# Performance work log

Hardware: AMD Instinct MI355X
Metric: run time of the kernel (lower is better)

Reference implementation:

```python
import jax, jax.numpy as jnp
import numpy as np

EPS = 1e-8  # torch.nn.CosineSimilarity default eps
SCALE_WEIGHT = (1.0, 2.0, 3.0, 4.0)  # weight[idx] for 4 scales


def _nearest_labels(lab, H, W):
    # torch F.interpolate mode='nearest': src_idx = floor(dst_idx * in/out)
    H0, W0 = lab.shape[2], lab.shape[3]
    ri = (jnp.arange(H) * H0) // H
    ci = (jnp.arange(W) * W0) // W
    return lab[:, :, ri][:, :, :, ci]


def _scale_loss(pseudo_labels, feat, feat_old, num_class, num_old_class):
    B, C, H, W = feat.shape
    lab = _nearest_labels(pseudo_labels, H, W).reshape(-1)          # [B*H*W]
    f = jnp.transpose(feat, (0, 2, 3, 1)).reshape(-1, C)            # (b h w) c
    fo = jnp.transpose(feat_old, (0, 2, 3, 1)).reshape(-1, C)
    nf = jnp.maximum(jnp.sqrt(jnp.sum(f * f, axis=1)), EPS)
    nfo = jnp.maximum(jnp.sqrt(jnp.sum(fo * fo, axis=1)), EPS)
    sim = jnp.sum(f * fo, axis=1) / (nf * nfo)                      # per-pixel cosine
    # segment-reduce by class; label 255 (ignore) is out-of-range and dropped
    seg = jax.ops.segment_sum(sim, lab, num_segments=num_class)
    cnt = jax.ops.segment_sum(jnp.ones_like(sim), lab, num_segments=num_class)
    mean_sim = seg / jnp.maximum(cnt, 1.0)
    cls = jnp.arange(num_class)
    factor = jnp.where(cls == 0, num_old_class / num_class,
                       jnp.where(cls <= num_old_class, 1.0, 0.0))
    present = cnt > 0
    dis = 1.0 - mean_sim
    return jnp.sum(jnp.where(present, factor * dis, 0.0))


def setup_inputs() -> dict:
    key = jax.random.key(0)
    ks = jax.random.split(key, 9)
    B, C = 8, 256
    sizes = [(128, 128), (64, 64), (32, 32), (16, 16)]
    inp = {
        "pseudo_labels": jax.random.randint(ks[0], (B, 1, 512, 512), 0, 21, dtype=jnp.int64)
        if jax.config.jax_enable_x64 else
        jax.random.randint(ks[0], (B, 1, 512, 512), 0, 21).astype(jnp.int32),
    }
    for i, (h, w) in enumerate(sizes):
        inp[f"f{i}"] = jax.random.normal(ks[1 + i], (B, C, h, w), dtype=jnp.float32)
        inp[f"fo{i}"] = jax.random.normal(ks[5 + i], (B, C, h, w), dtype=jnp.float32)
    inp["num_class"] = 21
    inp["num_old_class"] = 15
    return inp


def reference(pseudo_labels, f0, f1, f2, f3, fo0, fo1, fo2, fo3, num_class, num_old_class):
    feats = (f0, f1, f2, f3)
    feats_old = (fo0, fo1, fo2, fo3)
    loss = jnp.float32(0.0)
    for idx in range(4):
        loss = loss + SCALE_WEIGHT[idx] * _scale_loss(
            pseudo_labels, feats[idx], feats_old[idx], num_class, num_old_class)
    return loss
```

## Files before the change

### kernel.cpp

```cpp
#include <hip/hip_runtime.h>
#include <math.h>


#define EPSV 1e-8f

__global__ __launch_bounds__(512)
void msrd_main(const float* __restrict__ f0, const float* __restrict__ fo0,
               const float* __restrict__ f1, const float* __restrict__ fo1,
               const float* __restrict__ f2, const float* __restrict__ fo2,
               const float* __restrict__ f3, const float* __restrict__ fo3,
               const int*   __restrict__ labels,
               const int*   __restrict__ p_nclass,
               float* __restrict__ ws)
{
    int bid = blockIdx.x;
    int scale, lb, logW, logHW, sshift;
    const float *f, *fo;
    if (bid < 512)      { scale = 0; lb = bid;       f = f0; fo = fo0; logW = 7; logHW = 14; sshift = 2; }
    else if (bid < 640) { scale = 1; lb = bid - 512; f = f1; fo = fo1; logW = 6; logHW = 12; sshift = 3; }
    else if (bid < 672) { scale = 2; lb = bid - 640; f = f2; fo = fo2; logW = 5; logHW = 10; sshift = 4; }
    else                { scale = 3; lb = bid - 672; f = f3; fo = fo3; logW = 4; logHW = 8;  sshift = 5; }
    const int HW = 1 << logHW;
    const int W  = 1 << logW;

    const int tid  = threadIdx.x;
    const int wave = tid >> 6;
    const int lane = tid & 63;

    const int g   = lb * 64 + lane;
    const int pix = g << 2;
    const int b   = pix >> logHW;
    const int rem = pix & (HW - 1);

    const int c0 = wave * 32;
    const float4* __restrict__ fp  = (const float4*)(f  + (size_t)(b * 256 + c0) * HW + rem);
    const float4* __restrict__ fop = (const float4*)(fo + (size_t)(b * 256 + c0) * HW + rem);
    const int str4 = HW >> 2;

    float dx=0.f,dy=0.f,dz=0.f,dw=0.f;
    float ax=0.f,ay=0.f,az=0.f,aw=0.f;
    float bx=0.f,by=0.f,bz=0.f,bw=0.f;
    #pragma unroll 4
    for (int c = 0; c < 32; ++c) {
        float4 x = fp[c * str4];
        float4 y = fop[c * str4];
        dx = fmaf(x.x, y.x, dx); dy = fmaf(x.y, y.y, dy);
        dz = fmaf(x.z, y.z, dz); dw = fmaf(x.w, y.w, dw);
        ax = fmaf(x.x, x.x, ax); ay = fmaf(x.y, x.y, ay);
        az = fmaf(x.z, x.z, az); aw = fmaf(x.w, x.w, aw);
        bx = fmaf(y.x, y.x, bx); by = fmaf(y.y, y.y, by);
        bz = fmaf(y.z, y.z, bz); bw = fmaf(y.w, y.w, bw);
    }

    __shared__ float4 sD[8][64], sA[8][64], sB[8][64];
    __shared__ float bin_sim[32], bin_cnt[32];
    if (tid < 32) { bin_sim[tid] = 0.f; bin_cnt[tid] = 0.f; }
    sD[wave][lane] = make_float4(dx,dy,dz,dw);
    sA[wave][lane] = make_float4(ax,ay,az,aw);
    sB[wave][lane] = make_float4(bx,by,bz,bw);
    __syncthreads();

    if (wave == 0) {
        float4 D = sD[0][lane], A = sA[0][lane], Bv = sB[0][lane];
        #pragma unroll
        for (int w = 1; w < 8; ++w) {
            float4 t;
            t = sD[w][lane]; D.x += t.x; D.y += t.y; D.z += t.z; D.w += t.w;
            t = sA[w][lane]; A.x += t.x; A.y += t.y; A.z += t.z; A.w += t.w;
            t = sB[w][lane]; Bv.x += t.x; Bv.y += t.y; Bv.z += t.z; Bv.w += t.w;
        }
        const int nclass  = *p_nclass;
        const int labbase = b << 18;
        float Dv[4] = {D.x, D.y, D.z, D.w};
        float Av[4] = {A.x, A.y, A.z, A.w};
        float Bw[4] = {Bv.x, Bv.y, Bv.z, Bv.w};
        #pragma unroll
        for (int j = 0; j < 4; ++j) {
            float na  = fmaxf(sqrtf(Av[j]), EPSV);
            float nb  = fmaxf(sqrtf(Bw[j]), EPSV);
            float sim = Dv[j] / (na * nb);
            int p    = rem + j;
            int h    = p >> logW;
            int col  = p & (W - 1);
            int lidx = labbase + ((h << sshift) << 9) + (col << sshift);
            int lab  = labels[lidx];
            if ((unsigned)lab < (unsigned)nclass) {
                atomicAdd(&bin_sim[lab], sim);
                atomicAdd(&bin_cnt[lab], 1.0f);
            }
        }
    }
    __syncthreads();

    if (tid < 32) {
        float s = bin_sim[tid], c = bin_cnt[tid];
        if (s != 0.f || c != 0.f) {
            atomicAdd(&ws[scale * 64 + tid],      s);
            atomicAdd(&ws[scale * 64 + 32 + tid], c);
        }
    }
}

__global__ void msrd_final(const float* __restrict__ ws,
                           const int* __restrict__ p_nclass,
                           const int* __restrict__ p_nold,
                           float* __restrict__ out)
{
    if (threadIdx.x == 0 && blockIdx.x == 0) {
        const int nc = *p_nclass;
        const int no = *p_nold;
        const float wgt[4] = {1.f, 2.f, 3.f, 4.f};
        float loss = 0.f;
        for (int s = 0; s < 4; ++s) {
            float sl = 0.f;
            for (int c = 0; c < nc && c < 32; ++c) {
                float seg = ws[s * 64 + c];
                float cnt = ws[s * 64 + 32 + c];
                if (cnt > 0.f) {
                    float factor = (c == 0) ? (float)no / (float)nc
                                            : (c <= no ? 1.f : 0.f);
                    sl += factor * (1.f - seg / fmaxf(cnt, 1.f));
                }
            }
            loss += wgt[s] * sl;
        }
        out[0] = loss;
    }
}

extern "C" void kernel_launch(void* const* d_in, const int* in_sizes, int n_in,
                              void* d_out, int out_size, void* d_ws, size_t ws_size,
                              hipStream_t stream) {
    const int*   labels = (const int*)  d_in[0];
    const float* f0  = (const float*)d_in[1];
    const float* fo0 = (const float*)d_in[2];
    const float* f1  = (const float*)d_in[3];
    const float* fo1 = (const float*)d_in[4];
    const float* f2  = (const float*)d_in[5];
    const float* fo2 = (const float*)d_in[6];
    const float* f3  = (const float*)d_in[7];
    const float* fo3 = (const float*)d_in[8];
    const int* p_nclass = (const int*)d_in[9];
    const int* p_nold   = (const int*)d_in[10];
    float* out = (float*)d_out;
    float* ws  = (float*)d_ws;

    hipMemsetAsync(ws, 0, 4 * 64 * sizeof(float), stream);
    msrd_main<<<dim3(680), dim3(512), 0, stream>>>(f0, fo0, f1, fo1, f2, fo2, f3, fo3,
                                                   labels, p_nclass, ws);
    msrd_final<<<dim3(1), dim3(64), 0, stream>>>(ws, p_nclass, p_nold, out);
}
```

Baseline: 360.8 us.

## Split channels across half-waves and batch loads for more parallelism

Each block now covers 128 pixels instead of 256, and the grid grows to 1360 blocks. Each half-wave takes 16 of a wave's 32 channels, and the two halves are combined with a cross-lane shuffle. The loads are issued in batches of eight float4 per tensor before the FMAs to raise memory-level parallelism. The cost is a row segment per channel that is half as long, so less contiguous bytes per access, plus more blocks and more global atomics.

```diff
diff --git a/kernel.cpp b/kernel.cpp
--- a/kernel.cpp
+++ b/kernel.cpp
@@ -16,58 +16,79 @@
     int bid = blockIdx.x;
     int scale, lb, logW, logHW, sshift;
     const float *f, *fo;
-    if (bid < 512)      { scale = 0; lb = bid;       f = f0; fo = fo0; logW = 7; logHW = 14; sshift = 2; }
-    else if (bid < 640) { scale = 1; lb = bid - 512; f = f1; fo = fo1; logW = 6; logHW = 12; sshift = 3; }
-    else if (bid < 672) { scale = 2; lb = bid - 640; f = f2; fo = fo2; logW = 5; logHW = 10; sshift = 4; }
-    else                { scale = 3; lb = bid - 672; f = f3; fo = fo3; logW = 4; logHW = 8;  sshift = 5; }
+    if (bid < 1024)      { scale = 0; lb = bid;        f = f0; fo = fo0; logW = 7; logHW = 14; sshift = 2; }
+    else if (bid < 1280) { scale = 1; lb = bid - 1024; f = f1; fo = fo1; logW = 6; logHW = 12; sshift = 3; }
+    else if (bid < 1344) { scale = 2; lb = bid - 1280; f = f2; fo = fo2; logW = 5; logHW = 10; sshift = 4; }
+    else                 { scale = 3; lb = bid - 1344; f = f3; fo = fo3; logW = 4; logHW = 8;  sshift = 5; }
     const int HW = 1 << logHW;
     const int W  = 1 << logW;
 
     const int tid  = threadIdx.x;
     const int wave = tid >> 6;
     const int lane = tid & 63;
+    const int half = lane >> 5;
+    const int gi   = lane & 31;
 
-    const int g   = lb * 64 + lane;
+    const int g   = lb * 32 + gi;
     const int pix = g << 2;
     const int b   = pix >> logHW;
     const int rem = pix & (HW - 1);
 
-    const int c0 = wave * 32;
-    const float4* __restrict__ fp  = (const float4*)(f  + (size_t)(b * 256 + c0) * HW + rem);
-    const float4* __restrict__ fop = (const float4*)(fo + (size_t)(b * 256 + c0) * HW + rem);
-    const int str4 = HW >> 2;
+    const int c0 = wave * 32 + half * 16;
+    const float* __restrict__ fpb  = f  + (((size_t)(b * 256 + c0)) << logHW) + rem;
+    const float* __restrict__ fopb = fo + (((size_t)(b * 256 + c0)) << logHW) + rem;
 
     float dx=0.f,dy=0.f,dz=0.f,dw=0.f;
     float ax=0.f,ay=0.f,az=0.f,aw=0.f;
     float bx=0.f,by=0.f,bz=0.f,bw=0.f;
-    #pragma unroll 4
-    for (int c = 0; c < 32; ++c) {
-        float4 x = fp[c * str4];
-        float4 y = fop[c * str4];
-        dx = fmaf(x.x, y.x, dx); dy = fmaf(x.y, y.y, dy);
-        dz = fmaf(x.z, y.z, dz); dw = fmaf(x.w, y.w, dw);
-        ax = fmaf(x.x, x.x, ax); ay = fmaf(x.y, x.y, ay);
-        az = fmaf(x.z, x.z, az); aw = fmaf(x.w, x.w, aw);
-        bx = fmaf(y.x, y.x, bx); by = fmaf(y.y, y.y, by);
-        bz = fmaf(y.z, y.z, bz); bw = fmaf(y.w, y.w, bw);
+
+    #pragma unroll
+    for (int batch = 0; batch < 2; ++batch) {
+        float4 X[8], Y[8];
+        const size_t cb = (size_t)(batch * 8) << logHW;
+        #pragma unroll
+        for (int j = 0; j < 8; ++j)
+            X[j] = *(const float4*)(fpb + cb + ((size_t)j << logHW));
+        #pragma unroll
+        for (int j = 0; j < 8; ++j)
+            Y[j] = *(const float4*)(fopb + cb + ((size_t)j << logHW));
+        #pragma unroll
+        for (int j = 0; j < 8; ++j) {
+            float4 x = X[j], y = Y[j];
+            dx = fmaf(x.x, y.x, dx); dy = fmaf(x.y, y.y, dy);
+            dz = fmaf(x.z, y.z, dz); dw = fmaf(x.w, y.w, dw);
+            ax = fmaf(x.x, x.x, ax); ay = fmaf(x.y, x.y, ay);
+            az = fmaf(x.z, x.z, az); aw = fmaf(x.w, x.w, aw);
+            bx = fmaf(y.x, y.x, bx); by = fmaf(y.y, y.y, by);
+            bz = fmaf(y.z, y.z, bz); bw = fmaf(y.w, y.w, bw);
+        }
     }
 
-    __shared__ float4 sD[8][64], sA[8][64], sB[8][64];
+    dx += __shfl_xor(dx, 32); dy += __shfl_xor(dy, 32);
+    dz += __shfl_xor(dz, 32); dw += __shfl_xor(dw, 32);
+    ax += __shfl_xor(ax, 32); ay += __shfl_xor(ay, 32);
+    az += __shfl_xor(az, 32); aw += __shfl_xor(aw, 32);
+    bx += __shfl_xor(bx, 32); by += __shfl_xor(by, 32);
+    bz += __shfl_xor(bz, 32); bw += __shfl_xor(bw, 32);
+
+    __shared__ float4 sD[8][32], sA[8][32], sB[8][32];
     __shared__ float bin_sim[32], bin_cnt[32];
     if (tid < 32) { bin_sim[tid] = 0.f; bin_cnt[tid] = 0.f; }
-    sD[wave][lane] = make_float4(dx,dy,dz,dw);
-    sA[wave][lane] = make_float4(ax,ay,az,aw);
-    sB[wave][lane] = make_float4(bx,by,bz,bw);
+    if (half == 0) {
+        sD[wave][gi] = make_float4(dx,dy,dz,dw);
+        sA[wave][gi] = make_float4(ax,ay,az,aw);
+        sB[wave][gi] = make_float4(bx,by,bz,bw);
+    }
     __syncthreads();
 
-    if (wave == 0) {
-        float4 D = sD[0][lane], A = sA[0][lane], Bv = sB[0][lane];
+    if (tid < 32) {
+        float4 D = sD[0][gi], A = sA[0][gi], Bv = sB[0][gi];
         #pragma unroll
         for (int w = 1; w < 8; ++w) {
             float4 t;
-            t = sD[w][lane]; D.x += t.x; D.y += t.y; D.z += t.z; D.w += t.w;
-            t = sA[w][lane]; A.x += t.x; A.y += t.y; A.z += t.z; A.w += t.w;
-            t = sB[w][lane]; Bv.x += t.x; Bv.y += t.y; Bv.z += t.z; Bv.w += t.w;
+            t = sD[w][gi]; D.x += t.x; D.y += t.y; D.z += t.z; D.w += t.w;
+            t = sA[w][gi]; A.x += t.x; A.y += t.y; A.z += t.z; A.w += t.w;
+            t = sB[w][gi]; Bv.x += t.x; Bv.y += t.y; Bv.z += t.z; Bv.w += t.w;
         }
         const int nclass  = *p_nclass;
         const int labbase = b << 18;
@@ -146,7 +167,7 @@
     float* ws  = (float*)d_ws;
 
     hipMemsetAsync(ws, 0, 4 * 64 * sizeof(float), stream);
-    msrd_main<<<dim3(680), dim3(512), 0, stream>>>(f0, fo0, f1, fo1, f2, fo2, f3, fo3,
-                                                   labels, p_nclass, ws);
+    msrd_main<<<dim3(1360), dim3(512), 0, stream>>>(f0, fo0, f1, fo1, f2, fo2, f3, fo3,
+                                                    labels, p_nclass, ws);
     msrd_final<<<dim3(1), dim3(64), 0, stream>>>(ws, p_nclass, p_nold, out);
 }
```

Result: no change. 360.5 us (-0.1%).

## Stream feature channels through double-buffered LDS via global_load_lds

Applied to the files above, without the earlier changes.

Each block now covers 256 pixels with one thread per pixel. Feature channels are streamed in 8-channel chunks into double-buffered shared memory using direct global-to-LDS loads, and the next chunk is issued while the current one is consumed. The chunk start is rotated per block so blocks spread over different channel regions. This removes the cross-wave partial-sum reduction and overlaps memory latency with compute, at the cost of a barrier per chunk and smaller 256-thread blocks.

```diff
diff --git a/kernel.cpp b/kernel.cpp
--- a/kernel.cpp
+++ b/kernel.cpp
@@ -4,7 +4,14 @@
 
 #define EPSV 1e-8f
 
-__global__ __launch_bounds__(512)
+typedef const __attribute__((address_space(1))) void GV;
+typedef __attribute__((address_space(3))) void LV;
+
+__device__ __forceinline__ void gl_lds16(const float* gp, float* lp) {
+    __builtin_amdgcn_global_load_lds((GV*)gp, (LV*)lp, 16, 0, 0);
+}
+
+__global__ __launch_bounds__(256)
 void msrd_main(const float* __restrict__ f0, const float* __restrict__ fo0,
                const float* __restrict__ f1, const float* __restrict__ fo1,
                const float* __restrict__ f2, const float* __restrict__ fo2,
@@ -13,92 +20,91 @@
                const int*   __restrict__ p_nclass,
                float* __restrict__ ws)
 {
-    int bid = blockIdx.x;
-    int scale, lb, logW, logHW, sshift;
+    const int bid = blockIdx.x;
+    int scale, win, logW, logHW, sshift;
     const float *f, *fo;
-    if (bid < 512)      { scale = 0; lb = bid;       f = f0; fo = fo0; logW = 7; logHW = 14; sshift = 2; }
-    else if (bid < 640) { scale = 1; lb = bid - 512; f = f1; fo = fo1; logW = 6; logHW = 12; sshift = 3; }
-    else if (bid < 672) { scale = 2; lb = bid - 640; f = f2; fo = fo2; logW = 5; logHW = 10; sshift = 4; }
-    else                { scale = 3; lb = bid - 672; f = f3; fo = fo3; logW = 4; logHW = 8;  sshift = 5; }
-    const int HW = 1 << logHW;
-    const int W  = 1 << logW;
+    if (bid < 512)      { scale = 0; win = bid;       f = f0; fo = fo0; logW = 7; logHW = 14; sshift = 2; }
+    else if (bid < 640) { scale = 1; win = bid - 512; f = f1; fo = fo1; logW = 6; logHW = 12; sshift = 3; }
+    else if (bid < 672) { scale = 2; win = bid - 640; f = f2; fo = fo2; logW = 5; logHW = 10; sshift = 4; }
+    else                { scale = 3; win = bid - 672; f = f3; fo = fo3; logW = 4; logHW = 8;  sshift = 5; }
+    const int W = 1 << logW;
 
     const int tid  = threadIdx.x;
     const int wave = tid >> 6;
     const int lane = tid & 63;
 
-    const int g   = lb * 64 + lane;
-    const int pix = g << 2;
-    const int b   = pix >> logHW;
-    const int rem = pix & (HW - 1);
+    const int pxbase = win << 8;
+    const int b      = pxbase >> logHW;
+    const int wrem   = pxbase & ((1 << logHW) - 1);
 
-    const int c0 = wave * 32;
-    const float4* __restrict__ fp  = (const float4*)(f  + (size_t)(b * 256 + c0) * HW + rem);
-    const float4* __restrict__ fop = (const float4*)(fo + (size_t)(b * 256 + c0) * HW + rem);
-    const int str4 = HW >> 2;
+    __shared__ float lds[2][16][256];
+    __shared__ float bin_sim[32], bin_cnt[32];
+    if (tid < 32) { bin_sim[tid] = 0.f; bin_cnt[tid] = 0.f; }
 
-    float dx=0.f,dy=0.f,dz=0.f,dw=0.f;
-    float ax=0.f,ay=0.f,az=0.f,aw=0.f;
-    float bx=0.f,by=0.f,bz=0.f,bw=0.f;
-    #pragma unroll 4
-    for (int c = 0; c < 32; ++c) {
-        float4 x = fp[c * str4];
-        float4 y = fop[c * str4];
-        dx = fmaf(x.x, y.x, dx); dy = fmaf(x.y, y.y, dy);
-        dz = fmaf(x.z, y.z, dz); dw = fmaf(x.w, y.w, dw);
-        ax = fmaf(x.x, x.x, ax); ay = fmaf(x.y, x.y, ay);
-        az = fmaf(x.z, x.z, az); aw = fmaf(x.w, x.w, aw);
-        bx = fmaf(y.x, y.x, bx); by = fmaf(y.y, y.y, by);
-        bz = fmaf(y.z, y.z, bz); bw = fmaf(y.w, y.w, bw);
+    const size_t img_off = ((size_t)(b << 8)) << logHW;
+
+    const int   p0    = wave * 4;
+    const float* base0 = (p0 < 8) ? f : fo;
+    (void)base0;
+
+    float dot = 0.f, na2 = 0.f, nb2 = 0.f;
+
+    #define ISSUE(s, buf)                                                        \
+        {                                                                        \
+            const int chunk = ((s) + bid) & 31;                                  \
+            _Pragma("unroll")                                                    \
+            for (int k = 0; k < 4; ++k) {                                        \
+                const int p  = p0 + k;                                           \
+                const float* tb = (p < 8) ? f : fo;                              \
+                const int ch = chunk * 8 + (p & 7);                              \
+                const float* gp = tb + img_off + (((size_t)ch) << logHW)         \
+                                   + wrem + lane * 4;                            \
+                gl_lds16(gp, &lds[(buf)][p][0]);                                 \
+            }                                                                    \
+        }
+
+    ISSUE(0, 0);
+    __syncthreads();
+
+    #pragma unroll 1
+    for (int s = 0; s < 32; ++s) {
+        const int buf = s & 1;
+        if (s < 31) ISSUE(s + 1, buf ^ 1);
+        #pragma unroll
+        for (int c = 0; c < 8; ++c) {
+            const float x = lds[buf][c][tid];
+            const float y = lds[buf][8 + c][tid];
+            dot = fmaf(x, y, dot);
+            na2 = fmaf(x, x, na2);
+            nb2 = fmaf(y, y, nb2);
+        }
+        __syncthreads();
     }
 
-    __shared__ float4 sD[8][64], sA[8][64], sB[8][64];
-    __shared__ float bin_sim[32], bin_cnt[32];
-    if (tid < 32) { bin_sim[tid] = 0.f; bin_cnt[tid] = 0.f; }
-    sD[wave][lane] = make_float4(dx,dy,dz,dw);
-    sA[wave][lane] = make_float4(ax,ay,az,aw);
-    sB[wave][lane] = make_float4(bx,by,bz,bw);
-    __syncthreads();
+    const float na  = fmaxf(sqrtf(na2), EPSV);
+    const float nb  = fmaxf(sqrtf(nb2), EPSV);
+    const float sim = dot / (na * nb);
 
-    if (wave == 0) {
-        float4 D = sD[0][lane], A = sA[0][lane], Bv = sB[0][lane];
-        #pragma unroll
-        for (int w = 1; w < 8; ++w) {
-            float4 t;
-            t = sD[w][lane]; D.x += t.x; D.y += t.y; D.z += t.z; D.w += t.w;
-            t = sA[w][lane]; A.x += t.x; A.y += t.y; A.z += t.z; A.w += t.w;
-            t = sB[w][lane]; Bv.x += t.x; Bv.y += t.y; Bv.z += t.z; Bv.w += t.w;
-        }
-        const int nclass  = *p_nclass;
-        const int labbase = b << 18;
-        float Dv[4] = {D.x, D.y, D.z, D.w};
-        float Av[4] = {A.x, A.y, A.z, A.w};
-        float Bw[4] = {Bv.x, Bv.y, Bv.z, Bv.w};
-        #pragma unroll
-        for (int j = 0; j < 4; ++j) {
-            float na  = fmaxf(sqrtf(Av[j]), EPSV);
-            float nb  = fmaxf(sqrtf(Bw[j]), EPSV);
-            float sim = Dv[j] / (na * nb);
-            int p    = rem + j;
-            int h    = p >> logW;
-            int col  = p & (W - 1);
-            int lidx = labbase + ((h << sshift) << 9) + (col << sshift);
-            int lab  = labels[lidx];
-            if ((unsigned)lab < (unsigned)nclass) {
-                atomicAdd(&bin_sim[lab], sim);
-                atomicAdd(&bin_cnt[lab], 1.0f);
-            }
-        }
+    const int p   = wrem + tid;
+    const int h   = p >> logW;
+    const int col = p & (W - 1);
+    const int lidx = (b << 18) + ((h << sshift) << 9) + (col << sshift);
+    const int lab  = labels[lidx];
+    const int nclass = *p_nclass;
+    if ((unsigned)lab < (unsigned)nclass) {
+        atomicAdd(&bin_sim[lab], sim);
+        atomicAdd(&bin_cnt[lab], 1.0f);
     }
     __syncthreads();
 
     if (tid < 32) {
-        float s = bin_sim[tid], c = bin_cnt[tid];
-        if (s != 0.f || c != 0.f) {
-            atomicAdd(&ws[scale * 64 + tid],      s);
-            atomicAdd(&ws[scale * 64 + 32 + tid], c);
+        float sv = bin_sim[tid], cv = bin_cnt[tid];
+        if (sv != 0.f || cv != 0.f) {
+            atomicAdd(&ws[scale * 64 + tid],      sv);
+            atomicAdd(&ws[scale * 64 + 32 + tid], cv);
         }
     }
+    #undef ISSUE
 }
 
 __global__ void msrd_final(const float* __restrict__ ws,
@@ -146,7 +152,7 @@
     float* ws  = (float*)d_ws;
 
     hipMemsetAsync(ws, 0, 4 * 64 * sizeof(float), stream);
-    msrd_main<<<dim3(680), dim3(512), 0, stream>>>(f0, fo0, f1, fo1, f2, fo2, f3, fo3,
+    msrd_main<<<dim3(680), dim3(256), 0, stream>>>(f0, fo0, f1, fo1, f2, fo2, f3, fo3,
                                                    labels, p_nclass, ws);
     msrd_final<<<dim3(1), dim3(64), 0, stream>>>(ws, p_nclass, p_nold, out);
 }
```

Result: no change. 366.3 us (+1.5%).

## Split channel reduction into LDS-staged pass and separate label-binning pass

Applied to the files above, without the earlier changes.

The single fused kernel is replaced by two passes. The first loads channel slices with global_load_lds into double-buffered shared memory, accumulates per-pixel dot and norm partials over 32-channel chunks, and writes them to workspace. The second pass reduces the 8 chunk partials, computes cosine similarity and bins it by label. The aim is more memory-level parallelism and overlap of loads with compute, at the cost of extra workspace traffic (about 16MB of partials written and read back) and one more launch. The old kernel remains as a fallback when the workspace is too small.

```diff
diff --git a/kernel.cpp b/kernel.cpp
--- a/kernel.cpp
+++ b/kernel.cpp
@@ -4,14 +4,159 @@
 
 #define EPSV 1e-8f
 
+#define P_S1 3145728
+#define P_S2 3932160
+#define P_S3 4128768
+#define P_END 4177920
+#define WS_NEEDED ((256 + P_END) * sizeof(float))
+
+typedef const __attribute__((address_space(1))) void GV;
+typedef __attribute__((address_space(3))) void LV;
+
+__device__ __forceinline__ void gl_lds16(const float* gp, float* lp) {
+    __builtin_amdgcn_global_load_lds((GV*)gp, (LV*)lp, 16, 0, 0);
+}
+
+__global__ __launch_bounds__(256)
+void msrd_pass1(const float* __restrict__ f0, const float* __restrict__ fo0,
+                const float* __restrict__ f1, const float* __restrict__ fo1,
+                const float* __restrict__ f2, const float* __restrict__ fo2,
+                const float* __restrict__ f3, const float* __restrict__ fo3,
+                float* __restrict__ part)
+{
+    const int bid = blockIdx.x;
+    int idx, logT, logHW, P;  const float *f, *fo; float* pbase;
+    if (bid < 512)      { idx = bid;      logT=3; logHW=14; P=2048; f=f0; fo=fo0; pbase = part; }
+    else if (bid < 640) { idx = bid-512;  logT=1; logHW=12; P=2048; f=f1; fo=fo1; pbase = part + P_S1; }
+    else if (bid < 704) { idx = bid-640;  logT=0; logHW=10; P=1024; f=f2; fo=fo2; pbase = part + P_S2; }
+    else                { idx = bid-704;  logT=0; logHW=8;  P=256;  f=f3; fo=fo3; pbase = part + P_S3; }
+    const int chunk = idx & 7;
+    const int tile  = (idx >> 3) & ((1 << logT) - 1);
+    const int b     = idx >> (3 + logT);
+    const int bt    = (b << logT) + tile;
+
+    const int tid = threadIdx.x, wave = tid >> 6, lane = tid & 63;
+
+    __shared__ float stage[2][2][2048];
+
+    const size_t base_off = (((size_t)(b * 256 + chunk * 32)) << logHW)
+                          + (size_t)tile * P;
+    const int nI = P >> 8;
+
+    float dA[2][4], nA[2][4], nB[2][4];
+    #pragma unroll
+    for (int j = 0; j < 2; ++j)
+        for (int k = 0; k < 4; ++k) { dA[j][k]=0.f; nA[j][k]=0.f; nB[j][k]=0.f; }
+
+    #define ISSUE(s, bf) do {                                                    \
+        const size_t co = base_off + (((size_t)(s)) << logHW);                   \
+        for (int i = wave; i < nI; i += 4) {                                     \
+            gl_lds16(f  + co + i * 256 + lane * 4, &stage[bf][0][i * 256]);      \
+            gl_lds16(fo + co + i * 256 + lane * 4, &stage[bf][1][i * 256]);      \
+        } } while (0)
+
+    ISSUE(0, 0);
+    __syncthreads();
+
+    #pragma unroll 1
+    for (int s = 0; s < 32; ++s) {
+        const int buf = s & 1;
+        if (s < 31) ISSUE(s + 1, buf ^ 1);
+        #pragma unroll
+        for (int j = 0; j < 2; ++j) {
+            const int g = tid + (j << 8);
+            if ((g << 2) < P) {
+                float4 x = *(const float4*)&stage[buf][0][g << 2];
+                float4 y = *(const float4*)&stage[buf][1][g << 2];
+                dA[j][0]=fmaf(x.x,y.x,dA[j][0]); dA[j][1]=fmaf(x.y,y.y,dA[j][1]);
+                dA[j][2]=fmaf(x.z,y.z,dA[j][2]); dA[j][3]=fmaf(x.w,y.w,dA[j][3]);
+                nA[j][0]=fmaf(x.x,x.x,nA[j][0]); nA[j][1]=fmaf(x.y,x.y,nA[j][1]);
+                nA[j][2]=fmaf(x.z,x.z,nA[j][2]); nA[j][3]=fmaf(x.w,x.w,nA[j][3]);
+                nB[j][0]=fmaf(y.x,y.x,nB[j][0]); nB[j][1]=fmaf(y.y,y.y,nB[j][1]);
+                nB[j][2]=fmaf(y.z,y.z,nB[j][2]); nB[j][3]=fmaf(y.w,y.w,nB[j][3]);
+            }
+        }
+        __syncthreads();
+    }
+    #undef ISSUE
+
+    float* outb = pbase + (size_t)(bt * 8 + chunk) * 3 * P;
+    #pragma unroll
+    for (int j = 0; j < 2; ++j) {
+        const int g = tid + (j << 8);
+        if ((g << 2) < P) {
+            *(float4*)&outb[g << 2]           = make_float4(dA[j][0],dA[j][1],dA[j][2],dA[j][3]);
+            *(float4*)&outb[P + (g << 2)]     = make_float4(nA[j][0],nA[j][1],nA[j][2],nA[j][3]);
+            *(float4*)&outb[2 * P + (g << 2)] = make_float4(nB[j][0],nB[j][1],nB[j][2],nB[j][3]);
+        }
+    }
+}
+
+__global__ __launch_bounds__(256)
+void msrd_pass2(const float* __restrict__ part, const int* __restrict__ labels,
+                const int* __restrict__ p_nclass, float* __restrict__ bins)
+{
+    const int gid = blockIdx.x * 256 + threadIdx.x;
+    int scale, bt, g, logT, logW, sshift, P; const float* pbase;
+    if (gid < 32768)      { scale=0; int q=gid;         bt=q>>9; g=q&511; logT=3; logW=7; sshift=2; P=2048; pbase=part; }
+    else if (gid < 40960) { scale=1; int q=gid-32768;   bt=q>>9; g=q&511; logT=1; logW=6; sshift=3; P=2048; pbase=part+P_S1; }
+    else if (gid < 43008) { scale=2; int q=gid-40960;   bt=q>>8; g=q&255; logT=0; logW=5; sshift=4; P=1024; pbase=part+P_S2; }
+    else                  { scale=3; int q=gid-43008;   bt=q>>6; g=q&63;  logT=0; logW=4; sshift=5; P=256;  pbase=part+P_S3; }
+
+    __shared__ float bin_sim[32], bin_cnt[32];
+    if (threadIdx.x < 32) { bin_sim[threadIdx.x] = 0.f; bin_cnt[threadIdx.x] = 0.f; }
+    __syncthreads();
+
+    float D[4] = {0,0,0,0}, A[4] = {0,0,0,0}, Bv[4] = {0,0,0,0};
+    const float* pb = pbase + (size_t)bt * 8 * 3 * P;
+    #pragma unroll
+    for (int c = 0; c < 8; ++c) {
+        const float* cb = pb + (size_t)c * 3 * P;
+        float4 d = *(const float4*)&cb[g << 2];
+        float4 a = *(const float4*)&cb[P + (g << 2)];
+        float4 bb = *(const float4*)&cb[2 * P + (g << 2)];
+        D[0]+=d.x; D[1]+=d.y; D[2]+=d.z; D[3]+=d.w;
+        A[0]+=a.x; A[1]+=a.y; A[2]+=a.z; A[3]+=a.w;
+        Bv[0]+=bb.x; Bv[1]+=bb.y; Bv[2]+=bb.z; Bv[3]+=bb.w;
+    }
+
+    const int b    = bt >> logT;
+    const int tile = bt & ((1 << logT) - 1);
+    const int W    = 1 << logW;
+    const int nclass = *p_nclass;
+    #pragma unroll
+    for (int j = 0; j < 4; ++j) {
+        float na  = fmaxf(sqrtf(A[j]), EPSV);
+        float nb  = fmaxf(sqrtf(Bv[j]), EPSV);
+        float sim = D[j] / (na * nb);
+        int p    = tile * P + (g << 2) + j;
+        int h    = p >> logW;
+        int col  = p & (W - 1);
+        int lidx = (b << 18) + ((h << sshift) << 9) + (col << sshift);
+        int lab  = labels[lidx];
+        if ((unsigned)lab < (unsigned)nclass) {
+            atomicAdd(&bin_sim[lab], sim);
+            atomicAdd(&bin_cnt[lab], 1.0f);
+        }
+    }
+    __syncthreads();
+
+    if (threadIdx.x < 32) {
+        float sv = bin_sim[threadIdx.x], cv = bin_cnt[threadIdx.x];
+        if (sv != 0.f || cv != 0.f) {
+            atomicAdd(&bins[scale * 64 + threadIdx.x],      sv);
+            atomicAdd(&bins[scale * 64 + 32 + threadIdx.x], cv);
+        }
+    }
+}
+
 __global__ __launch_bounds__(512)
-void msrd_main(const float* __restrict__ f0, const float* __restrict__ fo0,
-               const float* __restrict__ f1, const float* __restrict__ fo1,
-               const float* __restrict__ f2, const float* __restrict__ fo2,
-               const float* __restrict__ f3, const float* __restrict__ fo3,
-               const int*   __restrict__ labels,
-               const int*   __restrict__ p_nclass,
-               float* __restrict__ ws)
+void msrd_fb(const float* __restrict__ f0, const float* __restrict__ fo0,
+             const float* __restrict__ f1, const float* __restrict__ fo1,
+             const float* __restrict__ f2, const float* __restrict__ fo2,
+             const float* __restrict__ f3, const float* __restrict__ fo3,
+             const int* __restrict__ labels, const int* __restrict__ p_nclass,
+             float* __restrict__ ws)
 {
     int bid = blockIdx.x;
     int scale, lb, logW, logHW, sshift;
@@ -20,70 +165,46 @@
     else if (bid < 640) { scale = 1; lb = bid - 512; f = f1; fo = fo1; logW = 6; logHW = 12; sshift = 3; }
     else if (bid < 672) { scale = 2; lb = bid - 640; f = f2; fo = fo2; logW = 5; logHW = 10; sshift = 4; }
     else                { scale = 3; lb = bid - 672; f = f3; fo = fo3; logW = 4; logHW = 8;  sshift = 5; }
-    const int HW = 1 << logHW;
-    const int W  = 1 << logW;
-
-    const int tid  = threadIdx.x;
-    const int wave = tid >> 6;
-    const int lane = tid & 63;
-
-    const int g   = lb * 64 + lane;
-    const int pix = g << 2;
-    const int b   = pix >> logHW;
-    const int rem = pix & (HW - 1);
-
-    const int c0 = wave * 32;
-    const float4* __restrict__ fp  = (const float4*)(f  + (size_t)(b * 256 + c0) * HW + rem);
-    const float4* __restrict__ fop = (const float4*)(fo + (size_t)(b * 256 + c0) * HW + rem);
+    const int HW = 1 << logHW, W = 1 << logW;
+    const int tid = threadIdx.x, wave = tid >> 6, lane = tid & 63;
+    const int pix = (lb * 64 + lane) << 2;
+    const int b = pix >> logHW, rem = pix & (HW - 1);
+    const float4* fp  = (const float4*)(f  + (size_t)(b * 256 + wave * 32) * HW + rem);
+    const float4* fop = (const float4*)(fo + (size_t)(b * 256 + wave * 32) * HW + rem);
     const int str4 = HW >> 2;
-
-    float dx=0.f,dy=0.f,dz=0.f,dw=0.f;
-    float ax=0.f,ay=0.f,az=0.f,aw=0.f;
-    float bx=0.f,by=0.f,bz=0.f,bw=0.f;
+    float dx=0,dy=0,dz=0,dw=0, ax=0,ay=0,az=0,aw=0, bx=0,by=0,bz=0,bw=0;
     #pragma unroll 4
     for (int c = 0; c < 32; ++c) {
-        float4 x = fp[c * str4];
-        float4 y = fop[c * str4];
-        dx = fmaf(x.x, y.x, dx); dy = fmaf(x.y, y.y, dy);
-        dz = fmaf(x.z, y.z, dz); dw = fmaf(x.w, y.w, dw);
-        ax = fmaf(x.x, x.x, ax); ay = fmaf(x.y, x.y, ay);
-        az = fmaf(x.z, x.z, az); aw = fmaf(x.w, x.w, aw);
-        bx = fmaf(y.x, y.x, bx); by = fmaf(y.y, y.y, by);
-        bz = fmaf(y.z, y.z, bz); bw = fmaf(y.w, y.w, bw);
-    }
-
+        float4 x = fp[c * str4], y = fop[c * str4];
+        dx=fmaf(x.x,y.x,dx); dy=fmaf(x.y,y.y,dy); dz=fmaf(x.z,y.z,dz); dw=fmaf(x.w,y.w,dw);
+        ax=fmaf(x.x,x.x,ax); ay=fmaf(x.y,x.y,ay); az=fmaf(x.z,x.z,az); aw=fmaf(x.w,x.w,aw);
+        bx=fmaf(y.x,y.x,bx); by=fmaf(y.y,y.y,by); bz=fmaf(y.z,y.z,bz); bw=fmaf(y.w,y.w,bw);
+    }
     __shared__ float4 sD[8][64], sA[8][64], sB[8][64];
     __shared__ float bin_sim[32], bin_cnt[32];
-    if (tid < 32) { bin_sim[tid] = 0.f; bin_cnt[tid] = 0.f; }
-    sD[wave][lane] = make_float4(dx,dy,dz,dw);
-    sA[wave][lane] = make_float4(ax,ay,az,aw);
-    sB[wave][lane] = make_float4(bx,by,bz,bw);
-    __syncthreads();
-
+    if (tid < 32) { bin_sim[tid]=0.f; bin_cnt[tid]=0.f; }
+    sD[wave][lane]=make_float4(dx,dy,dz,dw);
+    sA[wave][lane]=make_float4(ax,ay,az,aw);
+    sB[wave][lane]=make_float4(bx,by,bz,bw);
+    __syncthreads();
     if (wave == 0) {
-        float4 D = sD[0][lane], A = sA[0][lane], Bv = sB[0][lane];
+        float4 D=sD[0][lane], A=sA[0][lane], Bv=sB[0][lane];
         #pragma unroll
         for (int w = 1; w < 8; ++w) {
             float4 t;
-            t = sD[w][lane]; D.x += t.x; D.y += t.y; D.z += t.z; D.w += t.w;
-            t = sA[w][lane]; A.x += t.x; A.y += t.y; A.z += t.z; A.w += t.w;
-            t = sB[w][lane]; Bv.x += t.x; Bv.y += t.y; Bv.z += t.z; Bv.w += t.w;
-        }
-        const int nclass  = *p_nclass;
-        const int labbase = b << 18;
-        float Dv[4] = {D.x, D.y, D.z, D.w};
-        float Av[4] = {A.x, A.y, A.z, A.w};
-        float Bw[4] = {Bv.x, Bv.y, Bv.z, Bv.w};
+            t=sD[w][lane]; D.x+=t.x;D.y+=t.y;D.z+=t.z;D.w+=t.w;
+            t=sA[w][lane]; A.x+=t.x;A.y+=t.y;A.z+=t.z;A.w+=t.w;
+            t=sB[w][lane]; Bv.x+=t.x;Bv.y+=t.y;Bv.z+=t.z;Bv.w+=t.w;
+        }
+        const int nclass = *p_nclass;
+        float Dv[4]={D.x,D.y,D.z,D.w}, Av[4]={A.x,A.y,A.z,A.w}, Bw[4]={Bv.x,Bv.y,Bv.z,Bv.w};
         #pragma unroll
         for (int j = 0; j < 4; ++j) {
-            float na  = fmaxf(sqrtf(Av[j]), EPSV);
-            float nb  = fmaxf(sqrtf(Bw[j]), EPSV);
-            float sim = Dv[j] / (na * nb);
-            int p    = rem + j;
-            int h    = p >> logW;
-            int col  = p & (W - 1);
-            int lidx = labbase + ((h << sshift) << 9) + (col << sshift);
-            int lab  = labels[lidx];
+            float na=fmaxf(sqrtf(Av[j]),EPSV), nb=fmaxf(sqrtf(Bw[j]),EPSV);
+            float sim = Dv[j]/(na*nb);
+            int p=rem+j, h=p>>logW, col=p&(W-1);
+            int lidx=(b<<18)+((h<<sshift)<<9)+(col<<sshift);
+            int lab=labels[lidx];
             if ((unsigned)lab < (unsigned)nclass) {
                 atomicAdd(&bin_sim[lab], sim);
                 atomicAdd(&bin_cnt[lab], 1.0f);
@@ -91,17 +212,16 @@
         }
     }
     __syncthreads();
-
     if (tid < 32) {
-        float s = bin_sim[tid], c = bin_cnt[tid];
-        if (s != 0.f || c != 0.f) {
-            atomicAdd(&ws[scale * 64 + tid],      s);
-            atomicAdd(&ws[scale * 64 + 32 + tid], c);
-        }
-    }
-}
-
-__global__ void msrd_final(const float* __restrict__ ws,
+        float s=bin_sim[tid], c=bin_cnt[tid];
+        if (s!=0.f || c!=0.f) {
+            atomicAdd(&ws[scale*64+tid], s);
+            atomicAdd(&ws[scale*64+32+tid], c);
+        }
+    }
+}
+
+__global__ void msrd_final(const float* __restrict__ bins,
                            const int* __restrict__ p_nclass,
                            const int* __restrict__ p_nold,
                            float* __restrict__ out)
@@ -114,8 +234,8 @@
         for (int s = 0; s < 4; ++s) {
             float sl = 0.f;
             for (int c = 0; c < nc && c < 32; ++c) {
-                float seg = ws[s * 64 + c];
-                float cnt = ws[s * 64 + 32 + c];
+                float seg = bins[s * 64 + c];
+                float cnt = bins[s * 64 + 32 + c];
                 if (cnt > 0.f) {
                     float factor = (c == 0) ? (float)no / (float)nc
                                             : (c <= no ? 1.f : 0.f);
@@ -145,8 +265,14 @@
     float* out = (float*)d_out;
     float* ws  = (float*)d_ws;
 
-    hipMemsetAsync(ws, 0, 4 * 64 * sizeof(float), stream);
-    msrd_main<<<dim3(680), dim3(512), 0, stream>>>(f0, fo0, f1, fo1, f2, fo2, f3, fo3,
-                                                   labels, p_nclass, ws);
+    hipMemsetAsync(ws, 0, 256 * sizeof(float), stream);
+    if (ws_size >= WS_NEEDED) {
+        msrd_pass1<<<dim3(768), dim3(256), 0, stream>>>(f0, fo0, f1, fo1, f2, fo2, f3, fo3,
+                                                        ws + 256);
+        msrd_pass2<<<dim3(170), dim3(256), 0, stream>>>(ws + 256, labels, p_nclass, ws);
+    } else {
+        msrd_fb<<<dim3(680), dim3(512), 0, stream>>>(f0, fo0, f1, fo1, f2, fo2, f3, fo3,
+                                                     labels, p_nclass, ws);
+    }
     msrd_final<<<dim3(1), dim3(64), 0, stream>>>(ws, p_nclass, p_nold, out);
 }
```

New measurement: 370.6 us. +2.7%, slower.
